# Kernel tuning notes

Hardware: AMD Instinct MI355X
Metric: run time of the kernel (lower is better)

## Reference

```python
import jax, jax.numpy as jnp
import numpy as np

S, D = 1024, 4096  # MC samples, latent dim


def setup_inputs() -> dict:
    key = jax.random.key(0)
    k1, k2 = jax.random.split(key)
    theta = jax.random.normal(k1, (S, D), dtype=jnp.float32)
    mu = jnp.zeros((D,), dtype=jnp.float32)
    b = 0.1 * jax.random.normal(k2, (D,), dtype=jnp.float32)
    log_c = jnp.zeros((D,), dtype=jnp.float32)
    return {"theta": theta, "mu": mu, "b": b, "log_c": log_c}


def reference(theta, mu, b, log_c):
    """log q(theta) under N(mu, Sigma), Sigma = b b^T + diag(c^2).

    Faithful to torch: builds the dense DxD covariance and uses a full
    Cholesky-based MVN log-prob (same math as torch.distributions.MultivariateNormal).
    Returns log-probs of shape [S].
    """
    d = mu.shape[0]
    c = jax.nn.softplus(log_c) + 1e-4                 # get_c()
    cov = jnp.outer(b, b) + jnp.diag(c * c)           # [D, D]
    L = jnp.linalg.cholesky(cov)                      # [D, D] lower
    diff = theta - mu                                 # [S, D]
    # Solve L y = diff^T  -> Mahalanobis term ||y||^2 per sample
    y = jax.scipy.linalg.solve_triangular(L, diff.T, lower=True)  # [D, S]
    quad = jnp.sum(y * y, axis=0)                     # [S]
    logdet = 2.0 * jnp.sum(jnp.log(jnp.diagonal(L)))
    log_2pi = jnp.log(jnp.asarray(2.0 * np.pi, dtype=theta.dtype))
    return -0.5 * (quad + d * log_2pi + logdet)
```

## Files before the change

### kernel.cpp

```cpp
#include <hip/hip_runtime.h>
#include <math.h>

#define DIMS 4096
#define NSAMP 1024

__device__ __forceinline__ float softplus_f(float x) {
    return fmaxf(x, 0.0f) + log1pf(expf(-fabsf(x)));
}

__global__ __launch_bounds__(256) void nagvac_prep(
        const float* __restrict__ b,
        const float* __restrict__ log_c,
        float* __restrict__ ws) {
    __shared__ float red[2][4];
    const int tid = threadIdx.x;
    float beta = 0.0f, slog = 0.0f;
    const float4* b4 = (const float4*)b;
    const float4* l4 = (const float4*)log_c;
    float4* ic4 = (float4*)ws;
    float4* w4  = (float4*)(ws + DIMS);

    for (int j = 0; j < DIMS / 4 / 256; ++j) {
        int v = j * 256 + tid;
        float4 bv = b4[v];
        float4 lv = l4[v];
        float bb[4] = {bv.x, bv.y, bv.z, bv.w};
        float ll[4] = {lv.x, lv.y, lv.z, lv.w};
        float ic[4], ww[4];
        #pragma unroll
        for (int k = 0; k < 4; ++k) {
            float c  = softplus_f(ll[k]) + 1e-4f;
            float i2 = 1.0f / (c * c);
            ic[k] = i2;
            ww[k] = bb[k] * i2;
            beta += bb[k] * bb[k] * i2;
            slog += logf(c);
        }
        ic4[v] = make_float4(ic[0], ic[1], ic[2], ic[3]);
        w4[v]  = make_float4(ww[0], ww[1], ww[2], ww[3]);
    }

    #pragma unroll
    for (int off = 32; off > 0; off >>= 1) {
        beta += __shfl_down(beta, off);
        slog += __shfl_down(slog, off);
    }
    const int wave = tid >> 6, lane = tid & 63;
    if (lane == 0) { red[0][wave] = beta; red[1][wave] = slog; }
    __syncthreads();
    if (tid == 0) {
        float B = red[0][0] + red[0][1] + red[0][2] + red[0][3];
        float L = red[1][0] + red[1][1] + red[1][2] + red[1][3];
        ws[2 * DIMS]     = B;
        ws[2 * DIMS + 1] = 2.0f * L;
    }
}

__global__ __launch_bounds__(256) void nagvac_logq(
        const float* __restrict__ theta,
        const float* __restrict__ mu,
        const float* __restrict__ ws,
        float* __restrict__ out) {
    __shared__ float red[2][4];
    const int s = blockIdx.x;
    const int tid = threadIdx.x;

    const float4* th = (const float4*)(theta + (size_t)s * DIMS);
    const float4* m4 = (const float4*)mu;
    const float4* ic4 = (const float4*)ws;
    const float4* w4  = (const float4*)(ws + DIMS);

    float a1 = 0.0f, a2 = 0.0f;
    #pragma unroll
    for (int j = 0; j < DIMS / 4 / 256; ++j) {
        int v = j * 256 + tid;
        float4 t = th[v];
        float4 m = m4[v];
        float4 ic = ic4[v];
        float4 w  = w4[v];
        float dx = t.x - m.x, dy = t.y - m.y, dz = t.z - m.z, dw = t.w - m.w;
        a1 += dx * dx * ic.x + dy * dy * ic.y + dz * dz * ic.z + dw * dw * ic.w;
        a2 += dx * w.x + dy * w.y + dz * w.z + dw * w.w;
    }

    #pragma unroll
    for (int off = 32; off > 0; off >>= 1) {
        a1 += __shfl_down(a1, off);
        a2 += __shfl_down(a2, off);
    }
    const int wave = tid >> 6, lane = tid & 63;
    if (lane == 0) { red[0][wave] = a1; red[1][wave] = a2; }
    __syncthreads();
    if (tid == 0) {
        float s1 = red[0][0] + red[0][1] + red[0][2] + red[0][3];
        float s2 = red[1][0] + red[1][1] + red[1][2] + red[1][3];
        float beta = ws[2 * DIMS];
        float tsl  = ws[2 * DIMS + 1];
        float quad = s1 - s2 * s2 / (1.0f + beta);
        const float LOG2PI = 1.8378770664093453f;
        out[s] = -0.5f * (quad + (float)DIMS * LOG2PI + tsl + log1pf(beta));
    }
}

extern "C" void kernel_launch(void* const* d_in, const int* in_sizes, int n_in,
                              void* d_out, int out_size, void* d_ws, size_t ws_size,
                              hipStream_t stream) {
    const float* theta = (const float*)d_in[0];
    const float* mu    = (const float*)d_in[1];
    const float* b     = (const float*)d_in[2];
    const float* log_c = (const float*)d_in[3];
    float* out = (float*)d_out;
    float* ws  = (float*)d_ws;

    nagvac_prep<<<1, 256, 0, stream>>>(b, log_c, ws);
    nagvac_logq<<<NSAMP, 256, 0, stream>>>(theta, mu, ws, out);
}
```

Baseline: 76.60 us.

## Fuse prep into logq kernel, recompute per-dim terms per block, two samples per block

Merges the single-block prep kernel into the main kernel. Each block recomputes softplus, the inverse variance and the weight terms from b and log_c and processes two samples, so the recompute is shared across them. This removes the serial one-block prep launch and the workspace round trip, and uses fast exp/log/rcp intrinsics. In exchange every block does redundant transcendental work per dimension, and the grid is halved to 512 blocks.

```diff
diff --git a/kernel.cpp b/kernel.cpp
--- a/kernel.cpp
+++ b/kernel.cpp
@@ -3,102 +3,87 @@
 
 #define DIMS 4096
 #define NSAMP 1024
+#define SPB 2
+#define TPB 256
 
-__device__ __forceinline__ float softplus_f(float x) {
-    return fmaxf(x, 0.0f) + log1pf(expf(-fabsf(x)));
+__device__ __forceinline__ float fast_softplus(float x) {
+    return fmaxf(x, 0.0f) + __logf(1.0f + __expf(-fabsf(x)));
 }
 
-__global__ __launch_bounds__(256) void nagvac_prep(
+__global__ __launch_bounds__(TPB) void nagvac_fused(
+        const float* __restrict__ theta,
+        const float* __restrict__ mu,
         const float* __restrict__ b,
         const float* __restrict__ log_c,
-        float* __restrict__ ws) {
-    __shared__ float red[2][4];
+        float* __restrict__ out) {
+    __shared__ float red[6][4];
     const int tid = threadIdx.x;
-    float beta = 0.0f, slog = 0.0f;
+    const int s0  = blockIdx.x * SPB;
+
+    const float4* t0 = (const float4*)(theta + (size_t)s0 * DIMS);
+    const float4* t1 = (const float4*)(theta + (size_t)(s0 + 1) * DIMS);
+    const float4* m4 = (const float4*)mu;
     const float4* b4 = (const float4*)b;
     const float4* l4 = (const float4*)log_c;
-    float4* ic4 = (float4*)ws;
-    float4* w4  = (float4*)(ws + DIMS);
 
-    for (int j = 0; j < DIMS / 4 / 256; ++j) {
-        int v = j * 256 + tid;
+    float a1_0 = 0.f, a2_0 = 0.f, a1_1 = 0.f, a2_1 = 0.f;
+    float beta = 0.f, slog = 0.f;
+
+    #pragma unroll
+    for (int j = 0; j < DIMS / 4 / TPB; ++j) {
+        const int v = j * TPB + tid;
+        float4 ta = t0[v];
+        float4 tb = t1[v];
+        float4 m  = m4[v];
         float4 bv = b4[v];
         float4 lv = l4[v];
-        float bb[4] = {bv.x, bv.y, bv.z, bv.w};
-        float ll[4] = {lv.x, lv.y, lv.z, lv.w};
-        float ic[4], ww[4];
+        float tt0[4] = {ta.x, ta.y, ta.z, ta.w};
+        float tt1[4] = {tb.x, tb.y, tb.z, tb.w};
+        float mm[4]  = {m.x, m.y, m.z, m.w};
+        float bb[4]  = {bv.x, bv.y, bv.z, bv.w};
+        float ll[4]  = {lv.x, lv.y, lv.z, lv.w};
         #pragma unroll
         for (int k = 0; k < 4; ++k) {
-            float c  = softplus_f(ll[k]) + 1e-4f;
-            float i2 = 1.0f / (c * c);
-            ic[k] = i2;
-            ww[k] = bb[k] * i2;
-            beta += bb[k] * bb[k] * i2;
-            slog += logf(c);
+            float c  = fast_softplus(ll[k]) + 1e-4f;
+            float i2 = __builtin_amdgcn_rcpf(c * c);
+            float w  = bb[k] * i2;
+            beta += bb[k] * w;
+            slog += __logf(c);
+            float d0 = tt0[k] - mm[k];
+            float d1 = tt1[k] - mm[k];
+            a1_0 = fmaf(d0 * d0, i2, a1_0);
+            a2_0 = fmaf(d0, w, a2_0);
+            a1_1 = fmaf(d1 * d1, i2, a1_1);
+            a2_1 = fmaf(d1, w, a2_1);
         }
-        ic4[v] = make_float4(ic[0], ic[1], ic[2], ic[3]);
-        w4[v]  = make_float4(ww[0], ww[1], ww[2], ww[3]);
     }
 
+    float vals[6] = {a1_0, a2_0, a1_1, a2_1, beta, slog};
     #pragma unroll
-    for (int off = 32; off > 0; off >>= 1) {
-        beta += __shfl_down(beta, off);
-        slog += __shfl_down(slog, off);
+    for (int r = 0; r < 6; ++r) {
+        float v = vals[r];
+        #pragma unroll
+        for (int off = 32; off > 0; off >>= 1) v += __shfl_down(v, off);
+        vals[r] = v;
     }
     const int wave = tid >> 6, lane = tid & 63;
-    if (lane == 0) { red[0][wave] = beta; red[1][wave] = slog; }
+    if (lane == 0) {
+        #pragma unroll
+        for (int r = 0; r < 6; ++r) red[r][wave] = vals[r];
+    }
     __syncthreads();
-    if (tid == 0) {
-        float B = red[0][0] + red[0][1] + red[0][2] + red[0][3];
-        float L = red[1][0] + red[1][1] + red[1][2] + red[1][3];
-        ws[2 * DIMS]     = B;
-        ws[2 * DIMS + 1] = 2.0f * L;
-    }
-}
 
-__global__ __launch_bounds__(256) void nagvac_logq(
-        const float* __restrict__ theta,
-        const float* __restrict__ mu,
-        const float* __restrict__ ws,
-        float* __restrict__ out) {
-    __shared__ float red[2][4];
-    const int s = blockIdx.x;
-    const int tid = threadIdx.x;
-
-    const float4* th = (const float4*)(theta + (size_t)s * DIMS);
-    const float4* m4 = (const float4*)mu;
-    const float4* ic4 = (const float4*)ws;
-    const float4* w4  = (const float4*)(ws + DIMS);
-
-    float a1 = 0.0f, a2 = 0.0f;
-    #pragma unroll
-    for (int j = 0; j < DIMS / 4 / 256; ++j) {
-        int v = j * 256 + tid;
-        float4 t = th[v];
-        float4 m = m4[v];
-        float4 ic = ic4[v];
-        float4 w  = w4[v];
-        float dx = t.x - m.x, dy = t.y - m.y, dz = t.z - m.z, dw = t.w - m.w;
-        a1 += dx * dx * ic.x + dy * dy * ic.y + dz * dz * ic.z + dw * dw * ic.w;
-        a2 += dx * w.x + dy * w.y + dz * w.z + dw * w.w;
-    }
-
-    #pragma unroll
-    for (int off = 32; off > 0; off >>= 1) {
-        a1 += __shfl_down(a1, off);
-        a2 += __shfl_down(a2, off);
-    }
-    const int wave = tid >> 6, lane = tid & 63;
-    if (lane == 0) { red[0][wave] = a1; red[1][wave] = a2; }
-    __syncthreads();
-    if (tid == 0) {
-        float s1 = red[0][0] + red[0][1] + red[0][2] + red[0][3];
-        float s2 = red[1][0] + red[1][1] + red[1][2] + red[1][3];
-        float beta = ws[2 * DIMS];
-        float tsl  = ws[2 * DIMS + 1];
-        float quad = s1 - s2 * s2 / (1.0f + beta);
+    if (tid < SPB) {
+        float A1 = red[2 * tid + 0][0] + red[2 * tid + 0][1]
+                 + red[2 * tid + 0][2] + red[2 * tid + 0][3];
+        float A2 = red[2 * tid + 1][0] + red[2 * tid + 1][1]
+                 + red[2 * tid + 1][2] + red[2 * tid + 1][3];
+        float B  = red[4][0] + red[4][1] + red[4][2] + red[4][3];
+        float SL = red[5][0] + red[5][1] + red[5][2] + red[5][3];
+        float quad = A1 - A2 * A2 / (1.0f + B);
         const float LOG2PI = 1.8378770664093453f;
-        out[s] = -0.5f * (quad + (float)DIMS * LOG2PI + tsl + log1pf(beta));
+        out[s0 + tid] = -0.5f * (quad + (float)DIMS * LOG2PI
+                                 + 2.0f * SL + log1pf(B));
     }
 }
 
@@ -110,8 +95,6 @@
     const float* b     = (const float*)d_in[2];
     const float* log_c = (const float*)d_in[3];
     float* out = (float*)d_out;
-    float* ws  = (float*)d_ws;
 
-    nagvac_prep<<<1, 256, 0, stream>>>(b, log_c, ws);
-    nagvac_logq<<<NSAMP, 256, 0, stream>>>(theta, mu, ws, out);
+    nagvac_fused<<<NSAMP / SPB, TPB, 0, stream>>>(theta, mu, b, log_c, out);
 }
```

Result: faster. 70.92 us (-7.4%).
